# Kernel tuning notes

Hardware: AMD Instinct MI355X
Metric: run time of the kernel (lower is better)

The kernel has to match this reference:

```python
import jax, jax.numpy as jnp
import numpy as np

N_NODES = 100000
N_EDGES = 2000000


def setup_inputs() -> dict:
    key = jax.random.key(0)
    ks = jax.random.split(key, 8)
    x = jax.random.normal(ks[0], (N_NODES, 8), dtype=jnp.float32)
    edge_index = jax.random.randint(ks[1], (2, N_EDGES), 0, N_NODES, dtype=jnp.int64)
    W1 = jax.random.normal(ks[2], (8, 32), dtype=jnp.float32) * (1.0 / np.sqrt(8))
    b1 = jnp.zeros((32,), dtype=jnp.float32)
    W2 = jax.random.normal(ks[3], (32, 32), dtype=jnp.float32) * (1.0 / np.sqrt(32))
    b2 = jnp.zeros((32,), dtype=jnp.float32)
    Wf = jax.random.normal(ks[4], (32, 1), dtype=jnp.float32) * (1.0 / np.sqrt(32))
    bf = jnp.zeros((1,), dtype=jnp.float32)
    return {"x": x, "edge_index": edge_index, "W1": W1, "b1": b1,
            "W2": W2, "b2": b2, "Wf": Wf, "bf": bf}


def _gcn_conv(x, src, dst, norm, W, b, n_nodes):
    # x: [N, Fin] -> [N, Fout]; standard PyG GCNConv with self-loops + sym norm
    h = x @ W                                   # [N, Fout]
    msg = h[src] * norm[:, None]                # gather + scale, [E+N, Fout]
    out = jax.ops.segment_sum(msg, dst, num_segments=n_nodes)  # scatter-add
    return out + b


def reference(x, edge_index, W1, b1, W2, b2, Wf, bf):
    n = x.shape[0]
    loop = jnp.arange(n, dtype=edge_index.dtype)
    src = jnp.concatenate([edge_index[0], loop])
    dst = jnp.concatenate([edge_index[1], loop])
    # symmetric normalization: deg from target indices (incl. self-loops)
    deg = jax.ops.segment_sum(jnp.ones_like(dst, dtype=x.dtype), dst, num_segments=n)
    dis = jnp.where(deg > 0, jax.lax.rsqrt(jnp.maximum(deg, 1e-12)), 0.0)
    norm = dis[src] * dis[dst]                  # [E+N]

    h = jax.nn.relu(_gcn_conv(x, src, dst, norm, W1, b1, n))
    h = jax.nn.relu(_gcn_conv(h, src, dst, norm, W2, b2, n))
    return h @ Wf + bf                          # [N, 1]
```

## Files before the change

### kernel.cpp

```cpp
#include <hip/hip_runtime.h>
#include <hip/hip_fp16.h>


#define NBLK 256
#define SHIFT 8
#define BMASK 255
#define NBUCK 512

__global__ void k_hist(const int* __restrict__ dst, int* __restrict__ part, int E) {
    __shared__ int hist[NBUCK];
    int t = threadIdx.x;
    hist[t] = 0; hist[t + 256] = 0;
    __syncthreads();
    int E4 = E >> 2;
    int chunk4 = (E4 + NBLK - 1) / NBLK;
    int b = blockIdx.x;
    int s4 = b * chunk4;
    int e4 = min(s4 + chunk4, E4);
    const int4* dst4 = (const int4*)dst;
    for (int i = s4 + t; i < e4; i += 256) {
        int4 d = dst4[i];
        atomicAdd(&hist[d.x >> SHIFT], 1);
        atomicAdd(&hist[d.y >> SHIFT], 1);
        atomicAdd(&hist[d.z >> SHIFT], 1);
        atomicAdd(&hist[d.w >> SHIFT], 1);
    }
    if (b == NBLK - 1) {
        for (int e = (E4 << 2) + t; e < E; e += 256)
            atomicAdd(&hist[dst[e] >> SHIFT], 1);
    }
    __syncthreads();
    part[(size_t)t * NBLK + b] = hist[t];
    part[(size_t)(t + 256) * NBLK + b] = hist[t + 256];
}

__global__ void k_scanA(int* __restrict__ part, int* __restrict__ btot) {
    int t = threadIdx.x;
    int b = blockIdx.x * 4 + (t >> 6);
    int lane = t & 63;
    int4* p4 = (int4*)(part + (size_t)b * NBLK);
    int4 v = p4[lane];
    int ls = v.x + v.y + v.z + v.w;
    int s = ls;
#pragma unroll
    for (int off = 1; off < 64; off <<= 1) {
        int u = __shfl_up(s, off, 64);
        if (lane >= off) s += u;
    }
    int base = s - ls;
    int4 o;
    o.x = base;
    o.y = base + v.x;
    o.z = o.y + v.y;
    o.w = o.z + v.z;
    p4[lane] = o;
    if (lane == 63) btot[b] = s;
}

__global__ void k_scanB(const int* __restrict__ btot, int* __restrict__ bbase,
                        int* __restrict__ rowptr, int n, int E) {
    __shared__ int tmp[NBUCK];
    int t = threadIdx.x;
    int v = btot[t];
    tmp[t] = v;
    __syncthreads();
    for (int off = 1; off < NBUCK; off <<= 1) {
        int add = (t >= off) ? tmp[t - off] : 0;
        __syncthreads();
        tmp[t] += add;
        __syncthreads();
    }
    bbase[t] = tmp[t] - v;
    if (t == NBUCK - 1) bbase[NBUCK] = tmp[NBUCK - 1];
    if (t == 0) rowptr[n] = E;
}

__global__ void k_binA2(const int* __restrict__ src, const int* __restrict__ dst,
                        const int* __restrict__ part, const int* __restrict__ bbase,
                        int* __restrict__ bpair, int E) {
    __shared__ int cur[NBUCK];
    int t = threadIdx.x;
    int b = blockIdx.x;
    cur[t] = part[(size_t)t * NBLK + b] + bbase[t];
    __syncthreads();
    int E4 = E >> 2;
    int chunk4 = (E4 + NBLK - 1) / NBLK;
    int s4 = b * chunk4;
    int e4 = min(s4 + chunk4, E4);
    const int4* src4 = (const int4*)src;
    const int4* dst4 = (const int4*)dst;
    for (int i = s4 + t; i < e4; i += 512) {
        int4 s = src4[i];
        int4 d = dst4[i];
        int p0 = atomicAdd(&cur[d.x >> SHIFT], 1);
        bpair[p0] = (s.x << SHIFT) | (d.x & BMASK);
        int p1 = atomicAdd(&cur[d.y >> SHIFT], 1);
        bpair[p1] = (s.y << SHIFT) | (d.y & BMASK);
        int p2 = atomicAdd(&cur[d.z >> SHIFT], 1);
        bpair[p2] = (s.z << SHIFT) | (d.z & BMASK);
        int p3 = atomicAdd(&cur[d.w >> SHIFT], 1);
        bpair[p3] = (s.w << SHIFT) | (d.w & BMASK);
    }
    if (b == NBLK - 1) {
        for (int e = (E4 << 2) + t; e < E; e += 512) {
            int sv = src[e], dv = dst[e];
            int p = atomicAdd(&cur[dv >> SHIFT], 1);
            bpair[p] = (sv << SHIFT) | (dv & BMASK);
        }
    }
}

__global__ void k_fill2(const int* __restrict__ bpair, const int* __restrict__ bbase,
                        const float* __restrict__ x,
                        int* __restrict__ rowptr, float* __restrict__ dis,
                        unsigned int* __restrict__ xs16, int* __restrict__ col, int n) {
    __shared__ int cnt[256];
    __shared__ int tmp[256];
    __shared__ int cur[256];
    __shared__ float sdis[256];
    int b = blockIdx.x;
    int t = threadIdx.x;
    int start = bbase[b], end = bbase[b + 1];
    if (t < 256) cnt[t] = 0;
    __syncthreads();
    for (int i = start + t; i < end; i += 512)
        atomicAdd(&cnt[bpair[i] & BMASK], 1);
    __syncthreads();
    int v0 = (t < 256) ? cnt[t] : 0;
    if (t < 256) tmp[t] = v0;
    __syncthreads();
    for (int off = 1; off < 256; off <<= 1) {
        int add = (t < 256 && t >= off) ? tmp[t - off] : 0;
        __syncthreads();
        if (t < 256) tmp[t] += add;
        __syncthreads();
    }
    if (t < 256) {
        int v = (b << SHIFT) + t;
        if (v < n) {
            int r = start + tmp[t] - v0;
            rowptr[v] = r;
            cur[t] = r;
            float dv = rsqrtf(1.0f + (float)v0);
            dis[v] = dv;
            sdis[t] = dv;
        }
    }
    __syncthreads();
    int ubase = (b << SHIFT) * 4;
    int nu = n * 4;
    const float2* x2 = (const float2*)x;
    for (int i = t; i < 1024; i += 512) {
        int gi = ubase + i;
        if (gi < nu) {
            float d = sdis[i >> 2];
            float2 xv = x2[gi];
            __half2 h2 = __float22half2_rn(make_float2(xv.x * d, xv.y * d));
            xs16[gi] = *(unsigned int*)&h2;
        }
    }
    for (int i = start + t; i < end; i += 512) {
        int p = bpair[i];
        int pos = atomicAdd(&cur[p & BMASK], 1);
        col[pos] = p >> SHIFT;
    }
}

__global__ void k_g1b(const int* __restrict__ rowptr, const int* __restrict__ col,
                      const uint4* __restrict__ xs16u4, const float* __restrict__ dis,
                      const float* __restrict__ W1, const float* __restrict__ b1,
                      const float* __restrict__ W2, uint2* __restrict__ g16u2, int n) {
    __shared__ float sW1[256];
    __shared__ float sW2[1024];
    __shared__ float sh[4][8][36];
    int t = threadIdx.x;
    sW1[t] = W1[t];
    for (int i = t; i < 1024; i += 256) sW2[i] = W2[i];
    __syncthreads();
    int widx = t >> 6, lane = t & 63;
    int nd = lane >> 3, j = lane & 7;
    int v = (blockIdx.x * 4 + widx) * 8 + nd;
    float a0 = 0.f, a1 = 0.f, a2 = 0.f, a3 = 0.f,
          a4 = 0.f, a5 = 0.f, a6 = 0.f, a7 = 0.f;
    int r0 = 0, r1 = 0;
    if (v < n) { r0 = rowptr[v]; r1 = rowptr[v + 1]; }
    for (int i = r0 + j; i < r1; i += 8) {
        uint4 raw = xs16u4[col[i]];
        float2 f0 = __half22float2(*(const __half2*)&raw.x);
        float2 f1 = __half22float2(*(const __half2*)&raw.y);
        float2 f2 = __half22float2(*(const __half2*)&raw.z);
        float2 f3 = __half22float2(*(const __half2*)&raw.w);
        a0 += f0.x; a1 += f0.y; a2 += f1.x; a3 += f1.y;
        a4 += f2.x; a5 += f2.y; a6 += f3.x; a7 += f3.y;
    }
    if (j == 0 && v < n) {
        uint4 raw = xs16u4[v];
        float2 f0 = __half22float2(*(const __half2*)&raw.x);
        float2 f1 = __half22float2(*(const __half2*)&raw.y);
        float2 f2 = __half22float2(*(const __half2*)&raw.z);
        float2 f3 = __half22float2(*(const __half2*)&raw.w);
        a0 += f0.x; a1 += f0.y; a2 += f1.x; a3 += f1.y;
        a4 += f2.x; a5 += f2.y; a6 += f3.x; a7 += f3.y;
    }
#pragma unroll
    for (int m = 1; m < 8; m <<= 1) {
        a0 += __shfl_xor(a0, m, 64);
        a1 += __shfl_xor(a1, m, 64);
        a2 += __shfl_xor(a2, m, 64);
        a3 += __shfl_xor(a3, m, 64);
        a4 += __shfl_xor(a4, m, 64);
        a5 += __shfl_xor(a5, m, 64);
        a6 += __shfl_xor(a6, m, 64);
        a7 += __shfl_xor(a7, m, 64);
    }
    float dv = (v < n) ? dis[v] : 0.f;
    int f0i = j * 4;
    float h0 = 0.f, h1 = 0.f, h2 = 0.f, h3 = 0.f;
    {
        float ak[8] = {a0, a1, a2, a3, a4, a5, a6, a7};
#pragma unroll
        for (int k = 0; k < 8; ++k) {
            float4 w = *(const float4*)&sW1[k * 32 + f0i];
            h0 += ak[k] * w.x; h1 += ak[k] * w.y;
            h2 += ak[k] * w.z; h3 += ak[k] * w.w;
        }
    }
    h0 = fmaxf(dv * h0 + b1[f0i + 0], 0.f);
    h1 = fmaxf(dv * h1 + b1[f0i + 1], 0.f);
    h2 = fmaxf(dv * h2 + b1[f0i + 2], 0.f);
    h3 = fmaxf(dv * h3 + b1[f0i + 3], 0.f);
    *(float4*)&sh[widx][nd][f0i] = make_float4(h0, h1, h2, h3);
    const float4* hrow = (const float4*)&sh[widx][nd][0];
    float4 hr[8];
#pragma unroll
    for (int k4 = 0; k4 < 8; ++k4) hr[k4] = hrow[k4];
    float g0 = 0.f, g1 = 0.f, g2 = 0.f, g3 = 0.f;
#pragma unroll
    for (int k4 = 0; k4 < 8; ++k4) {
        float hk[4] = {hr[k4].x, hr[k4].y, hr[k4].z, hr[k4].w};
#pragma unroll
        for (int m = 0; m < 4; ++m) {
            float4 w = *(const float4*)&sW2[(k4 * 4 + m) * 32 + f0i];
            g0 += hk[m] * w.x; g1 += hk[m] * w.y;
            g2 += hk[m] * w.z; g3 += hk[m] * w.w;
        }
    }
    if (v < n) {
        __half2 ha = __float22half2_rn(make_float2(g0 * dv, g1 * dv));
        __half2 hb = __float22half2_rn(make_float2(g2 * dv, g3 * dv));
        uint2 o;
        o.x = *(unsigned int*)&ha;
        o.y = *(unsigned int*)&hb;
        g16u2[(size_t)v * 8 + j] = o;
    }
}

__global__ void k_g2f(const int* __restrict__ rowptr, const int* __restrict__ col,
                      const uint4* __restrict__ g16u4, const float* __restrict__ dis,
                      const float* __restrict__ b2, const float* __restrict__ Wf,
                      const float* __restrict__ bf, float* __restrict__ out, int n) {
    int t = threadIdx.x;
    int wave = t >> 6, lane = t & 63;
    int nd = lane >> 3, sub = lane & 7;
    int slot = sub >> 2, q = sub & 3;
    int v = (blockIdx.x * 4 + wave) * 8 + nd;
    if (v >= n) return;
    int r0 = rowptr[v], r1 = rowptr[v + 1];
    float4 s0 = make_float4(0.f, 0.f, 0.f, 0.f);
    float4 s1 = make_float4(0.f, 0.f, 0.f, 0.f);
    if (slot == 0) {
        uint4 raw = g16u4[(size_t)v * 4 + q];
        float2 f0 = __half22float2(*(const __half2*)&raw.x);
        float2 f1 = __half22float2(*(const __half2*)&raw.y);
        float2 f2 = __half22float2(*(const __half2*)&raw.z);
        float2 f3 = __half22float2(*(const __half2*)&raw.w);
        s0.x += f0.x; s0.y += f0.y; s0.z += f1.x; s0.w += f1.y;
        s1.x += f2.x; s1.y += f2.y; s1.z += f3.x; s1.w += f3.y;
    }
    for (int i = r0 + slot; i < r1; i += 2) {
        uint4 raw = g16u4[(size_t)col[i] * 4 + q];
        float2 f0 = __half22float2(*(const __half2*)&raw.x);
        float2 f1 = __half22float2(*(const __half2*)&raw.y);
        float2 f2 = __half22float2(*(const __half2*)&raw.z);
        float2 f3 = __half22float2(*(const __half2*)&raw.w);
        s0.x += f0.x; s0.y += f0.y; s0.z += f1.x; s0.w += f1.y;
        s1.x += f2.x; s1.y += f2.y; s1.z += f3.x; s1.w += f3.y;
    }
    s0.x += __shfl_xor(s0.x, 4, 64);
    s0.y += __shfl_xor(s0.y, 4, 64);
    s0.z += __shfl_xor(s0.z, 4, 64);
    s0.w += __shfl_xor(s0.w, 4, 64);
    s1.x += __shfl_xor(s1.x, 4, 64);
    s1.y += __shfl_xor(s1.y, 4, 64);
    s1.z += __shfl_xor(s1.z, 4, 64);
    s1.w += __shfl_xor(s1.w, 4, 64);
    float dv = dis[v];
    float4 bv0 = ((const float4*)b2)[q * 2], bv1 = ((const float4*)b2)[q * 2 + 1];
    float4 wv0 = ((const float4*)Wf)[q * 2], wv1 = ((const float4*)Wf)[q * 2 + 1];
    float p = fmaxf(dv * s0.x + bv0.x, 0.f) * wv0.x
            + fmaxf(dv * s0.y + bv0.y, 0.f) * wv0.y
            + fmaxf(dv * s0.z + bv0.z, 0.f) * wv0.z
            + fmaxf(dv * s0.w + bv0.w, 0.f) * wv0.w
            + fmaxf(dv * s1.x + bv1.x, 0.f) * wv1.x
            + fmaxf(dv * s1.y + bv1.y, 0.f) * wv1.y
            + fmaxf(dv * s1.z + bv1.z, 0.f) * wv1.z
            + fmaxf(dv * s1.w + bv1.w, 0.f) * wv1.w;
    p += __shfl_xor(p, 1, 64);
    p += __shfl_xor(p, 2, 64);
    if (sub == 0) out[v] = p + bf[0];
}

extern "C" void kernel_launch(void* const* d_in, const int* in_sizes, int n_in,
                              void* d_out, int out_size, void* d_ws, size_t ws_size,
                              hipStream_t stream) {
    const float* x  = (const float*)d_in[0];
    const int*   ei = (const int*)d_in[1];
    const float* W1 = (const float*)d_in[2];
    const float* b1 = (const float*)d_in[3];
    const float* W2 = (const float*)d_in[4];
    const float* b2 = (const float*)d_in[5];
    const float* Wf = (const float*)d_in[6];
    const float* bf = (const float*)d_in[7];
    float* out = (float*)d_out;

    const int n = in_sizes[0] / 8;
    const int E = in_sizes[1] / 2;
    const int* src = ei;
    const int* dst = ei + E;
    const int nbuck = (n + 255) >> 8;
    const size_t na = (size_t)((n + 3) & ~3);

    float* dis         = (float*)d_ws;
    unsigned int* xs16 = (unsigned int*)(dis + na);
    unsigned int* g16  = xs16 + na * 4;
    int* rowptr        = (int*)(g16 + na * 16);
    int* bbase         = rowptr + (n + 1);
    int* btot          = bbase + (NBUCK + 1);
    int* part          = btot + NBUCK + 2;
    int* col           = part + (size_t)NBUCK * NBLK;
    int* bpair         = col + E;

    k_hist <<<dim3(NBLK),      dim3(256), 0, stream>>>(dst, part, E);
    k_scanA<<<dim3(NBUCK / 4), dim3(256), 0, stream>>>(part, btot);
    k_scanB<<<dim3(1),         dim3(NBUCK), 0, stream>>>(btot, bbase, rowptr, n, E);
    k_binA2<<<dim3(NBLK),      dim3(512), 0, stream>>>(src, dst, part, bbase, bpair, E);
    k_fill2<<<dim3(nbuck),     dim3(512), 0, stream>>>(bpair, bbase, x, rowptr, dis, xs16, col, n);

    k_g1b<<<dim3((n + 31) / 32), dim3(256), 0, stream>>>(rowptr, col, (const uint4*)xs16,
                                                         dis, W1, b1, W2, (uint2*)g16, n);

    k_g2f<<<dim3((n + 31) / 32), dim3(256), 0, stream>>>(rowptr, col, (const uint4*)g16, dis,
                                                         b2, Wf, bf, out, n);
}
```

Measured before the change: 95.02 us.

## Split layer-2 gather by feature quarter across blocks with partial-sum reduction

The final aggregation kernel previously had 8 lanes per node (4 feature quarters × 2 edge slots). It now launches 4 separate blocks per node chunk, one per 8-feature quarter, with 2 lanes per node. Each block writes a partial output dot-product, and a new small kernel sums the four partials and adds the bias. The intent is to give more concurrent nodes per wave and better cache locality per quarter slice. The cost is re-reading rowptr and col four times, plus an extra kernel launch and a partial buffer round trip.

```diff
diff --git a/kernel.cpp b/kernel.cpp
--- a/kernel.cpp
+++ b/kernel.cpp
@@ -255,20 +255,21 @@
     }
 }
 
-__global__ void k_g2f(const int* __restrict__ rowptr, const int* __restrict__ col,
+__global__ void k_g2q(const int* __restrict__ rowptr, const int* __restrict__ col,
                       const uint4* __restrict__ g16u4, const float* __restrict__ dis,
                       const float* __restrict__ b2, const float* __restrict__ Wf,
-                      const float* __restrict__ bf, float* __restrict__ out, int n) {
+                      float* __restrict__ partial, int n) {
+    int q = blockIdx.x & 3;
+    int chunk = blockIdx.x >> 2;
     int t = threadIdx.x;
     int wave = t >> 6, lane = t & 63;
-    int nd = lane >> 3, sub = lane & 7;
-    int slot = sub >> 2, q = sub & 3;
-    int v = (blockIdx.x * 4 + wave) * 8 + nd;
+    int nd = lane >> 1, sub = lane & 1;
+    int v = chunk * 128 + wave * 32 + nd;
     if (v >= n) return;
     int r0 = rowptr[v], r1 = rowptr[v + 1];
     float4 s0 = make_float4(0.f, 0.f, 0.f, 0.f);
     float4 s1 = make_float4(0.f, 0.f, 0.f, 0.f);
-    if (slot == 0) {
+    if (sub == 0) {
         uint4 raw = g16u4[(size_t)v * 4 + q];
         float2 f0 = __half22float2(*(const __half2*)&raw.x);
         float2 f1 = __half22float2(*(const __half2*)&raw.y);
@@ -277,7 +278,7 @@
         s0.x += f0.x; s0.y += f0.y; s0.z += f1.x; s0.w += f1.y;
         s1.x += f2.x; s1.y += f2.y; s1.z += f3.x; s1.w += f3.y;
     }
-    for (int i = r0 + slot; i < r1; i += 2) {
+    for (int i = r0 + sub; i < r1; i += 2) {
         uint4 raw = g16u4[(size_t)col[i] * 4 + q];
         float2 f0 = __half22float2(*(const __half2*)&raw.x);
         float2 f1 = __half22float2(*(const __half2*)&raw.y);
@@ -286,28 +287,36 @@
         s0.x += f0.x; s0.y += f0.y; s0.z += f1.x; s0.w += f1.y;
         s1.x += f2.x; s1.y += f2.y; s1.z += f3.x; s1.w += f3.y;
     }
-    s0.x += __shfl_xor(s0.x, 4, 64);
-    s0.y += __shfl_xor(s0.y, 4, 64);
-    s0.z += __shfl_xor(s0.z, 4, 64);
-    s0.w += __shfl_xor(s0.w, 4, 64);
-    s1.x += __shfl_xor(s1.x, 4, 64);
-    s1.y += __shfl_xor(s1.y, 4, 64);
-    s1.z += __shfl_xor(s1.z, 4, 64);
-    s1.w += __shfl_xor(s1.w, 4, 64);
-    float dv = dis[v];
-    float4 bv0 = ((const float4*)b2)[q * 2], bv1 = ((const float4*)b2)[q * 2 + 1];
-    float4 wv0 = ((const float4*)Wf)[q * 2], wv1 = ((const float4*)Wf)[q * 2 + 1];
-    float p = fmaxf(dv * s0.x + bv0.x, 0.f) * wv0.x
-            + fmaxf(dv * s0.y + bv0.y, 0.f) * wv0.y
-            + fmaxf(dv * s0.z + bv0.z, 0.f) * wv0.z
-            + fmaxf(dv * s0.w + bv0.w, 0.f) * wv0.w
-            + fmaxf(dv * s1.x + bv1.x, 0.f) * wv1.x
-            + fmaxf(dv * s1.y + bv1.y, 0.f) * wv1.y
-            + fmaxf(dv * s1.z + bv1.z, 0.f) * wv1.z
-            + fmaxf(dv * s1.w + bv1.w, 0.f) * wv1.w;
-    p += __shfl_xor(p, 1, 64);
-    p += __shfl_xor(p, 2, 64);
-    if (sub == 0) out[v] = p + bf[0];
+    s0.x += __shfl_xor(s0.x, 1, 64);
+    s0.y += __shfl_xor(s0.y, 1, 64);
+    s0.z += __shfl_xor(s0.z, 1, 64);
+    s0.w += __shfl_xor(s0.w, 1, 64);
+    s1.x += __shfl_xor(s1.x, 1, 64);
+    s1.y += __shfl_xor(s1.y, 1, 64);
+    s1.z += __shfl_xor(s1.z, 1, 64);
+    s1.w += __shfl_xor(s1.w, 1, 64);
+    if (sub == 0) {
+        float dv = dis[v];
+        float4 bv0 = ((const float4*)b2)[q * 2], bv1 = ((const float4*)b2)[q * 2 + 1];
+        float4 wv0 = ((const float4*)Wf)[q * 2], wv1 = ((const float4*)Wf)[q * 2 + 1];
+        float p = fmaxf(dv * s0.x + bv0.x, 0.f) * wv0.x
+                + fmaxf(dv * s0.y + bv0.y, 0.f) * wv0.y
+                + fmaxf(dv * s0.z + bv0.z, 0.f) * wv0.z
+                + fmaxf(dv * s0.w + bv0.w, 0.f) * wv0.w
+                + fmaxf(dv * s1.x + bv1.x, 0.f) * wv1.x
+                + fmaxf(dv * s1.y + bv1.y, 0.f) * wv1.y
+                + fmaxf(dv * s1.z + bv1.z, 0.f) * wv1.z
+                + fmaxf(dv * s1.w + bv1.w, 0.f) * wv1.w;
+        partial[(size_t)q * n + v] = p;
+    }
+}
+
+__global__ void k_sum4(const float* __restrict__ partial, const float* __restrict__ bf,
+                       float* __restrict__ out, int n) {
+    int v = blockIdx.x * 256 + threadIdx.x;
+    if (v >= n) return;
+    out[v] = partial[v] + partial[(size_t)n + v] + partial[(size_t)2 * n + v]
+           + partial[(size_t)3 * n + v] + bf[0];
 }
 
 extern "C" void kernel_launch(void* const* d_in, const int* in_sizes, int n_in,
@@ -333,7 +342,8 @@
     float* dis         = (float*)d_ws;
     unsigned int* xs16 = (unsigned int*)(dis + na);
     unsigned int* g16  = xs16 + na * 4;
-    int* rowptr        = (int*)(g16 + na * 16);
+    float* partial     = (float*)(g16 + na * 16);
+    int* rowptr        = (int*)(partial + na * 4);
     int* bbase         = rowptr + (n + 1);
     int* btot          = bbase + (NBUCK + 1);
     int* part          = btot + NBUCK + 2;
@@ -349,6 +359,8 @@
     k_g1b<<<dim3((n + 31) / 32), dim3(256), 0, stream>>>(rowptr, col, (const uint4*)xs16,
                                                          dis, W1, b1, W2, (uint2*)g16, n);
 
-    k_g2f<<<dim3((n + 31) / 32), dim3(256), 0, stream>>>(rowptr, col, (const uint4*)g16, dis,
-                                                         b2, Wf, bf, out, n);
-}
+    const int nchunk = (n + 127) / 128;
+    k_g2q<<<dim3(4 * nchunk), dim3(256), 0, stream>>>(rowptr, col, (const uint4*)g16, dis,
+                                                      b2, Wf, partial, n);
+    k_sum4<<<dim3((n + 255) / 256), dim3(256), 0, stream>>>(partial, bf, out, n);
+}
```

New measurement: 191.4 us. +101.4%, slower.
